# Optimization experiments

Measured on AMD Instinct MI355X. Metric: run time of the kernel, lower is better.

Reference implementation:

```python
import jax, jax.numpy as jnp
import numpy as np

C, HEADS, K, P, S = 384, 12, 3, 1, 1
B, H, W = 8, 56, 56


def _unfold(v, k, p, s):
    # v: [B, C, Hs, Ws] -> [B, C, k*k, oh*ow], matching torch.nn.Unfold layout
    b, c, hs, ws = v.shape
    vp = jnp.pad(v, ((0, 0), (0, 0), (p, p), (p, p)))
    oh = (hs + 2 * p - k) // s + 1
    ow = (ws + 2 * p - k) // s + 1
    patches = jnp.stack(
        [vp[:, :, i:i + oh * s:s, j:j + ow * s:s] for i in range(k) for j in range(k)],
        axis=2,
    )  # [B, C, k*k, oh, ow]
    return patches.reshape(b, c, k * k, oh * ow)


def _fold(patches, out_h, out_w, k, p, s):
    # patches: [B, C, k*k, oh, ow] -> scatter-add to [B, C, out_h, out_w]
    b, c, _, oh, ow = patches.shape
    out = jnp.zeros((b, c, out_h + 2 * p, out_w + 2 * p), patches.dtype)
    for i in range(k):
        for j in range(k):
            out = out.at[:, :, i:i + oh * s:s, j:j + ow * s:s].add(patches[:, :, i * k + j])
    return out[:, :, p:p + out_h, p:p + out_w]


def setup_inputs() -> dict:
    key = jax.random.key(0)
    ks = jax.random.split(key, 6)
    sc = C ** -0.5
    return {
        "x": jax.random.normal(ks[0], (B, C, H, W), jnp.float32),
        "Wv": jax.random.normal(ks[1], (C, C), jnp.float32) * sc,
        "Wa": jax.random.normal(ks[2], (K ** 4 * HEADS, C), jnp.float32) * sc,
        "ba": jax.random.normal(ks[3], (K ** 4 * HEADS,), jnp.float32) * 0.01,
        "Wp": jax.random.normal(ks[4], (C, C), jnp.float32) * sc,
        "bp": jax.random.normal(ks[5], (C,), jnp.float32) * 0.01,
    }


def reference(x, Wv, Wa, ba, Wp, bp):
    b, c, h, w = x.shape
    hd = c // HEADS
    height = -(-h // S)
    width = -(-w // S)
    L = height * width
    x_hwc = x.transpose(0, 2, 3, 1)  # [B,H,W,C]
    # value projection, then the original's spatial transpose quirk: [B,C,W,H]
    v = jnp.einsum('bhwc,dc->bdwh', x_hwc, Wv)
    v = _unfold(v, K, P, S)  # [B, C, k*k, L]
    v = v.reshape(b, HEADS, hd, K * K, L).transpose(0, 1, 4, 3, 2)  # [B,n,L,k2,hd]
    # avgPool with kernel=stride=1 is identity
    a = jnp.einsum('bhwc,ec->bhwe', x_hwc, Wa) + ba
    a = a.reshape(b, L, HEADS, K * K, K * K).transpose(0, 2, 1, 3, 4)
    a = jax.nn.softmax(a * (hd ** -0.5), axis=-1)  # [B,n,L,k2,k2]
    out = jnp.einsum('bnlpq,bnlqd->bnlpd', a, v)  # [B,n,L,k2,hd]
    out = out.transpose(0, 1, 4, 3, 2).reshape(b, c, K * K, height, width)
    out = _fold(out, h, w, K, P, S)  # [B,C,H,W]
    out = jnp.einsum('bchw,dc->bhwd', out, Wp) + bp
    return out.transpose(0, 3, 1, 2)
```

## Files before the change

kernel.cpp:

```cpp
#include <hip/hip_runtime.h>
#include <hip/hip_bf16.h>
#include <math.h>

#define BATCH 8
#define CIN   384
#define HEADS 12
#define HGT   56
#define WID   56
#define HW    3136
#define NPIX  (BATCH*HW)
#define NVAL  384
#define NATT_W 1152
#define NQKV  1536
#define KSTEPS (CIN/32)

typedef __bf16 bf16x8 __attribute__((ext_vector_type(8)));
typedef __bf16 bf16x4 __attribute__((ext_vector_type(4)));
typedef float f32x4 __attribute__((ext_vector_type(4)));
typedef __hip_bfloat16 hbf16;

__device__ __forceinline__ void gload_lds16(const void* g, void* l) {
  __builtin_amdgcn_global_load_lds(
      (const __attribute__((address_space(1))) void*)g,
      (__attribute__((address_space(3))) void*)l, 16, 0, 0);
}

#define NB_CONVX 9408
#define NB_WQKV  2304
#define NB_WP    576
__global__ __launch_bounds__(256) void prep_all(
    const float* __restrict__ x,
    const float* __restrict__ Wv, const float* __restrict__ Wa,
    const float* __restrict__ ba, const float* __restrict__ Wp,
    hbf16* __restrict__ xb, hbf16* __restrict__ wcat,
    float* __restrict__ bcat, hbf16* __restrict__ wpb)
{
  const int bid = blockIdx.x;
  const int tid = threadIdx.x;
  if (bid < NB_CONVX) {
    __shared__ float s[32][33];
    const int xt = bid % 98;
    const int yt = (bid / 98) % 12;
    const int b  = bid / (98 * 12);
    const int hw0 = xt * 32, c0 = yt * 32;
    const int tx = tid & 31, ty = tid >> 5;
    #pragma unroll
    for (int i = 0; i < 4; i++) {
      int c = c0 + ty + i * 8;
      s[ty + i * 8][tx] = x[((size_t)b * CIN + c) * HW + hw0 + tx];
    }
    __syncthreads();
    #pragma unroll
    for (int i = 0; i < 4; i++) {
      int hw = hw0 + ty + i * 8;
      xb[((size_t)b * HW + hw) * CIN + c0 + tx] =
          __float2bfloat16(s[tx][ty + i * 8]);
    }
  } else if (bid < NB_CONVX + NB_WQKV) {
    const int i = (bid - NB_CONVX) * 256 + tid;
    if (i < NQKV * CIN) {
      int n = i / CIN, k = i % CIN;
      float v = 0.f;
      if (n < NVAL) {
        v = Wv[(size_t)n * CIN + k];
      } else {
        int a = n - NVAL;
        int head = a / 96, r = a % 96, p = r / 10, q = r % 10;
        if (p < 9 && q < 9)
          v = Wa[(size_t)(head * 81 + p * 9 + q) * CIN + k];
      }
      wcat[i] = __float2bfloat16(v);
    }
    if (i < NQKV) {
      float bv = 0.f;
      if (i >= NVAL) {
        int a = i - NVAL;
        int head = a / 96, r = a % 96, p = r / 10, q = r % 10;
        if (p < 9 && q < 9) bv = ba[head * 81 + p * 9 + q];
      }
      bcat[i] = bv;
    }
  } else {
    const int i = (bid - NB_CONVX - NB_WQKV) * 256 + tid;
    if (i < CIN * CIN) wpb[i] = __float2bfloat16(Wp[i]);
  }
}

template<int MODE>
__global__ __launch_bounds__(256, 4) void gemm_fused(
    const hbf16* __restrict__ A_,
    const hbf16* __restrict__ Bt_,
    const float* __restrict__ bias,
    hbf16* __restrict__ ovp,
    hbf16* __restrict__ oat,
    float* __restrict__ oput)
{
  __shared__ __align__(16) char smem[33280];
  const __bf16* A  = (const __bf16*)A_;
  const __bf16* Bt = (const __bf16*)Bt_;

  const int tid  = threadIdx.x;
  const int wave = tid >> 6, lane = tid & 63;
  const int wr = wave >> 1, wc = wave & 1;
  const int l16 = lane & 15, kg = lane >> 4;
  const int m0 = blockIdx.x * 128, n0 = blockIdx.y * 128;

  float* biasLds = (float*)(smem + 32768);
  if (tid < 128) biasLds[tid] = bias[n0 + tid];

  const int srow = tid >> 2;
  const int skb  = (tid & 3) * 16;

  f32x4 acc[4][4] = {};

  auto stage = [&](int k0, int buf) {
    const char* gA = (const char*)(A  + (size_t)m0 * CIN + k0);
    const char* gB = (const char*)(Bt + (size_t)n0 * CIN + k0);
    char* lA = smem + buf * 16384;
    char* lB = smem + buf * 16384 + 8192;
    #pragma unroll
    for (int p = 0; p < 2; p++) {
      int row = p * 64 + srow;
      gload_lds16(gA + (size_t)row * (CIN * 2) + skb, lA + p * 4096 + wave * 1024);
      gload_lds16(gB + (size_t)row * (CIN * 2) + skb, lB + p * 4096 + wave * 1024);
    }
  };

  stage(0, 0);
  __syncthreads();

  for (int t = 0; t < KSTEPS; ++t) {
    const int buf = t & 1;
    if (t + 1 < KSTEPS) stage((t + 1) * 32, buf ^ 1);

    const __bf16* As = (const __bf16*)(smem + buf * 16384);
    const __bf16* Bs = (const __bf16*)(smem + buf * 16384 + 8192);
    bf16x8 af[4], bfr[4];
    #pragma unroll
    for (int mi = 0; mi < 4; mi++)
      af[mi] = *(const bf16x8*)(As + (wr * 64 + mi * 16 + l16) * 32 + kg * 8);
    #pragma unroll
    for (int ni = 0; ni < 4; ni++)
      bfr[ni] = *(const bf16x8*)(Bs + (wc * 64 + ni * 16 + l16) * 32 + kg * 8);
    #pragma unroll
    for (int mi = 0; mi < 4; mi++)
      #pragma unroll
      for (int ni = 0; ni < 4; ni++) {
        if (MODE == 0)
          acc[ni][mi] = __builtin_amdgcn_mfma_f32_16x16x32_bf16(
              bfr[ni], af[mi], acc[ni][mi], 0, 0, 0);
        else
          acc[mi][ni] = __builtin_amdgcn_mfma_f32_16x16x32_bf16(
              af[mi], bfr[ni], acc[mi][ni], 0, 0, 0);
      }
    __syncthreads();
  }

  if (MODE == 0) {
    __bf16* epi = (__bf16*)smem;
    #pragma unroll
    for (int ni = 0; ni < 4; ni++) {
      #pragma unroll
      for (int mi = 0; mi < 4; mi++) {
        const int m  = wr * 64 + mi * 16 + l16;
        const int nb = wc * 64 + ni * 16 + kg * 4;
        bf16x4 v4;
        #pragma unroll
        for (int r = 0; r < 4; r++)
          v4[r] = (__bf16)__float2bfloat16(acc[ni][mi][r] + biasLds[nb + r]);
        *(bf16x4*)(epi + m * 128 + (nb ^ ((m & 7) << 3))) = v4;
      }
    }
    __syncthreads();
    const bool isv = (n0 < NVAL);
    #pragma unroll
    for (int q = 0; q < 8; q++) {
      const int cid = q * 256 + tid;
      const int m = cid >> 4, nc = cid & 15;
      const int nloc = nc * 8;
      bf16x8 v = *(const bf16x8*)(epi + m * 128 + (nloc ^ ((m & 7) << 3)));
      const int mg = m0 + m;
      if (isv)
        *(bf16x8*)(ovp + (size_t)mg * NVAL + n0 + nloc) = v;
      else
        *(bf16x8*)(oat + (size_t)mg * NATT_W + (n0 - NVAL) + nloc) = v;
    }
  } else {
    float* epi = (float*)smem;
    #pragma unroll
    for (int p = 0; p < 2; p++) {
      if (p) __syncthreads();
      if (wr == p) {
        #pragma unroll
        for (int mi = 0; mi < 4; mi++) {
          #pragma unroll
          for (int ni = 0; ni < 4; ni++) {
            const int n  = wc * 64 + ni * 16 + l16;
            const int ml = mi * 16 + kg * 4;
            f32x4 v;
            #pragma unroll
            for (int r = 0; r < 4; r++) v[r] = acc[mi][ni][r] + biasLds[n];
            *(f32x4*)(epi + n * 64 + (ml ^ ((n & 7) << 2))) = v;
          }
        }
      }
      __syncthreads();
      #pragma unroll
      for (int q = 0; q < 8; q++) {
        const int cid = q * 256 + tid;
        const int n = cid >> 4, mc = cid & 15;
        const int ml = mc * 4;
        f32x4 v = *(const f32x4*)(epi + n * 64 + (ml ^ ((n & 7) << 2)));
        const int mg = m0 + p * 64 + ml;
        const int b = mg / HW, hw = mg % HW;
        *(f32x4*)(oput + ((size_t)b * NVAL + n0 + n) * HW + hw) = v;
      }
    }
  }
}

__global__ __launch_bounds__(256) void fold_fused(
    const hbf16* __restrict__ attnb,
    const hbf16* __restrict__ vprojb,
    hbf16* __restrict__ foldedb)
{
  __shared__ float Wl[4][4 * HEADS * 25];

  const int b    = blockIdx.x & 7;
  const int tile = blockIdx.x >> 3;
  const int tx = tile % 14, ty = tile / 14;
  const int bofs = b * HW;
  const int tid = threadIdx.x;
  const int w    = tid >> 6;
  const int lane = tid & 63;
  const int x0 = tx * 4 + (w & 1) * 2;
  const int y0 = ty * 4 + (w >> 1) * 2;
  const bool interior = (tx >= 1) && (tx <= 12) && (ty >= 1) && (ty <= 12);
  const float scale = 0.17677669529663687f;

  if (lane < 48) {
    const int pixL = lane / HEADS, head = lane - pixL * HEADS;
    const int y = y0 + (pixL >> 1), x = x0 + (pixL & 1);

    float W[25];
    #pragma unroll
    for (int k = 0; k < 25; k++) W[k] = 0.f;

    auto docenter = [&](int i, int j) {
      const uint32_t* rp = (const uint32_t*)(attnb +
          (size_t)(bofs + (y - i + 1) * WID + (x - j + 1)) * NATT_W +
          head * 96 + (i * 3 + j) * 10);
      float v[9];
      #pragma unroll
      for (int u = 0; u < 4; u++) {
        uint32_t bits = rp[u];
        v[2 * u]     = __uint_as_float(bits << 16) * scale;
        v[2 * u + 1] = __uint_as_float(bits & 0xffff0000u) * scale;
      }
      v[8] = __uint_as_float(rp[4] << 16) * scale;
      float m = -1e30f;
      #pragma unroll
      for (int q = 0; q < 9; q++) m = fmaxf(m, v[q]);
      float s = 0.f;
      #pragma unroll
      for (int q = 0; q < 9; q++) { v[q] = __expf(v[q] - m); s += v[q]; }
      const float inv = 1.f / s;
      #pragma unroll
      for (int ip = 0; ip < 3; ip++)
        #pragma unroll
        for (int jp = 0; jp < 3; jp++)
          W[(ip - i + 2) * 5 + (jp - j + 2)] += v[ip * 3 + jp] * inv;
    };

    if (interior) {
      #pragma unroll
      for (int i = 0; i < 3; i++)
        #pragma unroll
        for (int j = 0; j < 3; j++)
          docenter(i, j);
    } else {
      #pragma unroll
      for (int i = 0; i < 3; i++)
        #pragma unroll
        for (int j = 0; j < 3; j++) {
          const int hh = y - i + 1, ww = x - j + 1;
          if (hh >= 0 && hh < HGT && ww >= 0 && ww < WID) docenter(i, j);
        }
    }
    float* o = &Wl[w][(pixL * HEADS + head) * 25];
    #pragma unroll
    for (int k = 0; k < 25; k++) o[k] = W[k];
  }

  asm volatile("s_waitcnt lgkmcnt(0)" ::: "memory");
  __builtin_amdgcn_wave_barrier();

  const int pixL = lane >> 4;
  const int ch16 = lane & 15;
  const int y = y0 + (pixL >> 1), x = x0 + (pixL & 1);
  const size_t pixofs = (size_t)(bofs + y * WID + x);
  const hbf16* vb0 = vprojb + (size_t)(bofs + (x - 2) * WID + (y - 2)) * NVAL;

  #pragma unroll
  for (int it = 0; it < 3; it++) {
    const int c0 = ch16 * 8 + it * 128;
    const int head = c0 >> 5;
    const float* Wp = &Wl[w][(pixL * HEADS + head) * 25];
    float acc[8];
    #pragma unroll
    for (int k = 0; k < 8; k++) acc[k] = 0.f;

    if (interior) {
      #pragma unroll
      for (int a = 0; a < 5; a++)
        #pragma unroll
        for (int e = 0; e < 5; e++) {
          const float w_ = Wp[a * 5 + e];
          const uint32_t* v = (const uint32_t*)(vb0 + (e * WID + a) * NVAL + c0);
          uint32_t b0 = v[0], b1 = v[1], b2 = v[2], b3 = v[3];
          acc[0] += w_ * __uint_as_float(b0 << 16);
          acc[1] += w_ * __uint_as_float(b0 & 0xffff0000u);
          acc[2] += w_ * __uint_as_float(b1 << 16);
          acc[3] += w_ * __uint_as_float(b1 & 0xffff0000u);
          acc[4] += w_ * __uint_as_float(b2 << 16);
          acc[5] += w_ * __uint_as_float(b2 & 0xffff0000u);
          acc[6] += w_ * __uint_as_float(b3 << 16);
          acc[7] += w_ * __uint_as_float(b3 & 0xffff0000u);
        }
    } else {
      #pragma unroll
      for (int a = 0; a < 5; a++) {
        const int wi = y + a - 2;
        #pragma unroll
        for (int e = 0; e < 5; e++) {
          const int hi = x + e - 2;
          if (wi >= 0 && wi < WID && hi >= 0 && hi < HGT) {
            const float w_ = Wp[a * 5 + e];
            const uint32_t* v = (const uint32_t*)(
                vprojb + (size_t)(bofs + hi * WID + wi) * NVAL + c0);
            uint32_t b0 = v[0], b1 = v[1], b2 = v[2], b3 = v[3];
            acc[0] += w_ * __uint_as_float(b0 << 16);
            acc[1] += w_ * __uint_as_float(b0 & 0xffff0000u);
            acc[2] += w_ * __uint_as_float(b1 << 16);
            acc[3] += w_ * __uint_as_float(b1 & 0xffff0000u);
            acc[4] += w_ * __uint_as_float(b2 << 16);
            acc[5] += w_ * __uint_as_float(b2 & 0xffff0000u);
            acc[6] += w_ * __uint_as_float(b3 << 16);
            acc[7] += w_ * __uint_as_float(b3 & 0xffff0000u);
          }
        }
      }
    }

    bf16x8 o;
    #pragma unroll
    for (int k = 0; k < 8; k++) o[k] = (__bf16)__float2bfloat16(acc[k]);
    *(bf16x8*)(foldedb + pixofs * NVAL + c0) = o;
  }
}

extern "C" void kernel_launch(void* const* d_in, const int* in_sizes, int n_in,
                              void* d_out, int out_size, void* d_ws, size_t ws_size,
                              hipStream_t stream)
{
  const float* x  = (const float*)d_in[0];
  const float* Wv = (const float*)d_in[1];
  const float* Wa = (const float*)d_in[2];
  const float* ba = (const float*)d_in[3];
  const float* Wp = (const float*)d_in[4];
  const float* bp = (const float*)d_in[5];
  float* out = (float*)d_out;

  char* w = (char*)d_ws;
  const size_t ATTN_B  = (size_t)NPIX * NATT_W * 2;
  const size_t VPROJ_B = (size_t)NPIX * NVAL * 2;
  const size_t XB_B    = (size_t)NPIX * CIN * 2;
  hbf16* attnb  = (hbf16*)w;
  hbf16* vprojb = (hbf16*)(w + ATTN_B);
  hbf16* xb     = (hbf16*)(w + ATTN_B + VPROJ_B);
  hbf16* wcat   = (hbf16*)(w + ATTN_B + VPROJ_B + XB_B);
  hbf16* wpb    = wcat + (size_t)NQKV * CIN;
  float* bcat   = (float*)(wpb + (size_t)CIN * CIN);
  hbf16* foldedb = xb;

  prep_all<<<dim3(NB_CONVX + NB_WQKV + NB_WP), 256, 0, stream>>>(
      x, Wv, Wa, ba, Wp, xb, wcat, bcat, wpb);
  gemm_fused<0><<<dim3(NPIX / 128, NQKV / 128), 256, 0, stream>>>(
      xb, wcat, bcat, vprojb, attnb, nullptr);
  fold_fused<<<dim3(8 * 196), 256, 0, stream>>>(attnb, vprojb, foldedb);
  gemm_fused<1><<<dim3(NPIX / 128, NVAL / 128), 256, 0, stream>>>(
      foldedb, wpb, bp, nullptr, nullptr, out);
}
```

Measured before the change: 129.6 us.

## Swizzle GEMM block order and compute fold softmax per center pixel

The GEMM launches become 1D grids with a remapped block order: groups of 8 M-blocks sweep all N-blocks together, with a tail path for the leftover M-blocks. This is meant to improve L2 reuse of A tiles across XCDs. The fold kernel now computes each center pixel's 9 softmaxes once per 4x4 tile, using a 6x6 halo with vectorized 16-byte loads. Results are accumulated into a shared 16-pixel weight table with LDS atomics, replacing per-pixel recomputation of every neighbour's softmax. This cuts redundant global reads and exp work, at the cost of LDS zeroing, atomics and an extra block barrier.

New measurement: 228.3 us. 76.1% more time.

```diff
diff --git a/kernel.cpp b/kernel.cpp
--- a/kernel.cpp
+++ b/kernel.cpp
@@ -13,10 +13,12 @@
 #define NATT_W 1152
 #define NQKV  1536
 #define KSTEPS (CIN/32)
+#define MB_TOT 196
 
 typedef __bf16 bf16x8 __attribute__((ext_vector_type(8)));
 typedef __bf16 bf16x4 __attribute__((ext_vector_type(4)));
 typedef float f32x4 __attribute__((ext_vector_type(4)));
+typedef uint32_t u32x4 __attribute__((ext_vector_type(4)));
 typedef __hip_bfloat16 hbf16;
 
 __device__ __forceinline__ void gload_lds16(const void* g, void* l) {
@@ -103,7 +105,23 @@
   const int wave = tid >> 6, lane = tid & 63;
   const int wr = wave >> 1, wc = wave & 1;
   const int l16 = lane & 15, kg = lane >> 4;
-  const int m0 = blockIdx.x * 128, n0 = blockIdx.y * 128;
+
+  const int NBN   = (MODE == 0) ? (NQKV / 128) : (NVAL / 128);
+  const int FULLB = 8 * NBN * (MB_TOT / 8);
+  int mb, nb;
+  {
+    const int wgid = blockIdx.x;
+    if (wgid < FULLB) {
+      const int xc = wgid & 7, r = wgid >> 3;
+      nb = r % NBN;
+      mb = (r / NBN) * 8 + xc;
+    } else {
+      const int l = wgid - FULLB;
+      nb = l >> 2;
+      mb = (MB_TOT & ~7) + (l & 3);
+    }
+  }
+  const int m0 = mb * 128, n0 = nb * 128;
 
   float* biasLds = (float*)(smem + 32768);
   if (tid < 128) biasLds[tid] = bias[n0 + tid];
@@ -163,12 +181,12 @@
       #pragma unroll
       for (int mi = 0; mi < 4; mi++) {
         const int m  = wr * 64 + mi * 16 + l16;
-        const int nb = wc * 64 + ni * 16 + kg * 4;
+        const int nb2 = wc * 64 + ni * 16 + kg * 4;
         bf16x4 v4;
         #pragma unroll
         for (int r = 0; r < 4; r++)
-          v4[r] = (__bf16)__float2bfloat16(acc[ni][mi][r] + biasLds[nb + r]);
-        *(bf16x4*)(epi + m * 128 + (nb ^ ((m & 7) << 3))) = v4;
+          v4[r] = (__bf16)__float2bfloat16(acc[ni][mi][r] + biasLds[nb2 + r]);
+        *(bf16x4*)(epi + m * 128 + (nb2 ^ ((m & 7) << 3))) = v4;
       }
     }
     __syncthreads();
@@ -224,88 +242,79 @@
     const hbf16* __restrict__ vprojb,
     hbf16* __restrict__ foldedb)
 {
-  __shared__ float Wl[4][4 * HEADS * 25];
+  __shared__ float Wl[16 * HEADS * 25];
 
   const int b    = blockIdx.x & 7;
   const int tile = blockIdx.x >> 3;
   const int tx = tile % 14, ty = tile / 14;
+  const int x0 = tx * 4, y0 = ty * 4;
   const int bofs = b * HW;
   const int tid = threadIdx.x;
-  const int w    = tid >> 6;
-  const int lane = tid & 63;
-  const int x0 = tx * 4 + (w & 1) * 2;
-  const int y0 = ty * 4 + (w >> 1) * 2;
+  const float scale = 0.17677669529663687f;
+
+  for (int i = tid; i < 16 * HEADS * 25; i += 256) Wl[i] = 0.f;
+  __syncthreads();
+
+  for (int u = tid; u < 36 * HEADS; u += 256) {
+    const int cpL = u / HEADS, head = u - cpL * HEADS;
+    const int cy = y0 + (cpL / 6) - 1;
+    const int cx = x0 + (cpL % 6) - 1;
+    if (cy < 0 || cy >= HGT || cx < 0 || cx >= WID) continue;
+
+    const u32x4* base = (const u32x4*)(attnb +
+        (size_t)(bofs + cy * WID + cx) * NATT_W + head * 96);
+    u32x4 dv[12];
+    #pragma unroll
+    for (int k = 0; k < 12; k++) dv[k] = base[k];
+
+    #pragma unroll
+    for (int r = 0; r < 9; r++) {
+      const int i = r / 3, j = r % 3;
+      const int py = cy + i - 1, px = cx + j - 1;
+      if (py >= y0 && py < y0 + 4 && px >= x0 && px < x0 + 4) {
+        float v[9];
+        #pragma unroll
+        for (int t = 0; t < 4; t++) {
+          const int k = 5 * r + t;
+          const uint32_t bits = dv[k >> 2][k & 3];
+          v[2 * t]     = __uint_as_float(bits << 16) * scale;
+          v[2 * t + 1] = __uint_as_float(bits & 0xffff0000u) * scale;
+        }
+        {
+          const int k = 5 * r + 4;
+          v[8] = __uint_as_float(dv[k >> 2][k & 3] << 16) * scale;
+        }
+        float m = -1e30f;
+        #pragma unroll
+        for (int q = 0; q < 9; q++) m = fmaxf(m, v[q]);
+        float s = 0.f;
+        #pragma unroll
+        for (int q = 0; q < 9; q++) { v[q] = __expf(v[q] - m); s += v[q]; }
+        const float inv = 1.f / s;
+        const int pixL = (py - y0) * 4 + (px - x0);
+        float* wp = &Wl[(pixL * HEADS + head) * 25];
+        #pragma unroll
+        for (int ip = 0; ip < 3; ip++)
+          #pragma unroll
+          for (int jp = 0; jp < 3; jp++)
+            atomicAdd(&wp[(ip - i + 2) * 5 + (jp - j + 2)], v[ip * 3 + jp] * inv);
+      }
+    }
+  }
+  __syncthreads();
+
+  const int pixL = tid >> 4;
+  const int ch16 = tid & 15;
+  const int y = y0 + (pixL >> 2), x = x0 + (pixL & 3);
+  const size_t pixofs = (size_t)(bofs + y * WID + x);
   const bool interior = (tx >= 1) && (tx <= 12) && (ty >= 1) && (ty <= 12);
-  const float scale = 0.17677669529663687f;
-
-  if (lane < 48) {
-    const int pixL = lane / HEADS, head = lane - pixL * HEADS;
-    const int y = y0 + (pixL >> 1), x = x0 + (pixL & 1);
-
-    float W[25];
-    #pragma unroll
-    for (int k = 0; k < 25; k++) W[k] = 0.f;
-
-    auto docenter = [&](int i, int j) {
-      const uint32_t* rp = (const uint32_t*)(attnb +
-          (size_t)(bofs + (y - i + 1) * WID + (x - j + 1)) * NATT_W +
-          head * 96 + (i * 3 + j) * 10);
-      float v[9];
-      #pragma unroll
-      for (int u = 0; u < 4; u++) {
-        uint32_t bits = rp[u];
-        v[2 * u]     = __uint_as_float(bits << 16) * scale;
-        v[2 * u + 1] = __uint_as_float(bits & 0xffff0000u) * scale;
-      }
-      v[8] = __uint_as_float(rp[4] << 16) * scale;
-      float m = -1e30f;
-      #pragma unroll
-      for (int q = 0; q < 9; q++) m = fmaxf(m, v[q]);
-      float s = 0.f;
-      #pragma unroll
-      for (int q = 0; q < 9; q++) { v[q] = __expf(v[q] - m); s += v[q]; }
-      const float inv = 1.f / s;
-      #pragma unroll
-      for (int ip = 0; ip < 3; ip++)
-        #pragma unroll
-        for (int jp = 0; jp < 3; jp++)
-          W[(ip - i + 2) * 5 + (jp - j + 2)] += v[ip * 3 + jp] * inv;
-    };
-
-    if (interior) {
-      #pragma unroll
-      for (int i = 0; i < 3; i++)
-        #pragma unroll
-        for (int j = 0; j < 3; j++)
-          docenter(i, j);
-    } else {
-      #pragma unroll
-      for (int i = 0; i < 3; i++)
-        #pragma unroll
-        for (int j = 0; j < 3; j++) {
-          const int hh = y - i + 1, ww = x - j + 1;
-          if (hh >= 0 && hh < HGT && ww >= 0 && ww < WID) docenter(i, j);
-        }
-    }
-    float* o = &Wl[w][(pixL * HEADS + head) * 25];
-    #pragma unroll
-    for (int k = 0; k < 25; k++) o[k] = W[k];
-  }
-
-  asm volatile("s_waitcnt lgkmcnt(0)" ::: "memory");
-  __builtin_amdgcn_wave_barrier();
-
-  const int pixL = lane >> 4;
-  const int ch16 = lane & 15;
-  const int y = y0 + (pixL >> 1), x = x0 + (pixL & 1);
-  const size_t pixofs = (size_t)(bofs + y * WID + x);
   const hbf16* vb0 = vprojb + (size_t)(bofs + (x - 2) * WID + (y - 2)) * NVAL;
 
   #pragma unroll
   for (int it = 0; it < 3; it++) {
     const int c0 = ch16 * 8 + it * 128;
     const int head = c0 >> 5;
-    const float* Wp = &Wl[w][(pixL * HEADS + head) * 25];
+    const float* Wp = &Wl[(pixL * HEADS + head) * 25];
     float acc[8];
     #pragma unroll
     for (int k = 0; k < 8; k++) acc[k] = 0.f;
@@ -385,9 +394,9 @@
 
   prep_all<<<dim3(NB_CONVX + NB_WQKV + NB_WP), 256, 0, stream>>>(
       x, Wv, Wa, ba, Wp, xb, wcat, bcat, wpb);
-  gemm_fused<0><<<dim3(NPIX / 128, NQKV / 128), 256, 0, stream>>>(
+  gemm_fused<0><<<dim3(MB_TOT * (NQKV / 128)), 256, 0, stream>>>(
       xb, wcat, bcat, vprojb, attnb, nullptr);
   fold_fused<<<dim3(8 * 196), 256, 0, stream>>>(attnb, vprojb, foldedb);
-  gemm_fused<1><<<dim3(NPIX / 128, NVAL / 128), 256, 0, stream>>>(
+  gemm_fused<1><<<dim3(MB_TOT * (NVAL / 128)), 256, 0, stream>>>(
       foldedb, wpb, bp, nullptr, nullptr, out);
 }
```

## Remap GEMM workgroups for XCD locality and widen fold tile to whole block

Applied to the files above, without the earlier changes.

The GEMM launches become a 1D grid with a custom block-id mapping that groups 8 consecutive M-blocks with all N-blocks, likely so that workgroups sharing A rows land on the same XCD/L2. The fold kernel now lets one block process a 4x4 pixel tile: 192 threads compute the softmax-fold weights for all 16 pixels, and the block uses a __syncthreads instead of per-wave 2x2 tiles. This shares the weight computation across the block, at the cost of idling 64 threads during the weight phase and adding a block-wide barrier.

After: 121.6 us. -6.2%, faster.

```diff
diff --git a/kernel.cpp b/kernel.cpp
--- a/kernel.cpp
+++ b/kernel.cpp
@@ -13,6 +13,7 @@
 #define NATT_W 1152
 #define NQKV  1536
 #define KSTEPS (CIN/32)
+#define MB_TOT 196
 
 typedef __bf16 bf16x8 __attribute__((ext_vector_type(8)));
 typedef __bf16 bf16x4 __attribute__((ext_vector_type(4)));
@@ -103,7 +104,23 @@
   const int wave = tid >> 6, lane = tid & 63;
   const int wr = wave >> 1, wc = wave & 1;
   const int l16 = lane & 15, kg = lane >> 4;
-  const int m0 = blockIdx.x * 128, n0 = blockIdx.y * 128;
+
+  const int NBN   = (MODE == 0) ? (NQKV / 128) : (NVAL / 128);
+  const int FULLB = 8 * NBN * (MB_TOT / 8);
+  int mb, nb;
+  {
+    const int wgid = blockIdx.x;
+    if (wgid < FULLB) {
+      const int xc = wgid & 7, r = wgid >> 3;
+      nb = r % NBN;
+      mb = (r / NBN) * 8 + xc;
+    } else {
+      const int l = wgid - FULLB;
+      nb = l >> 2;
+      mb = (MB_TOT & ~7) + (l & 3);
+    }
+  }
+  const int m0 = mb * 128, n0 = nb * 128;
 
   float* biasLds = (float*)(smem + 32768);
   if (tid < 128) biasLds[tid] = bias[n0 + tid];
@@ -163,12 +180,12 @@
       #pragma unroll
       for (int mi = 0; mi < 4; mi++) {
         const int m  = wr * 64 + mi * 16 + l16;
-        const int nb = wc * 64 + ni * 16 + kg * 4;
+        const int nb2 = wc * 64 + ni * 16 + kg * 4;
         bf16x4 v4;
         #pragma unroll
         for (int r = 0; r < 4; r++)
-          v4[r] = (__bf16)__float2bfloat16(acc[ni][mi][r] + biasLds[nb + r]);
-        *(bf16x4*)(epi + m * 128 + (nb ^ ((m & 7) << 3))) = v4;
+          v4[r] = (__bf16)__float2bfloat16(acc[ni][mi][r] + biasLds[nb2 + r]);
+        *(bf16x4*)(epi + m * 128 + (nb2 ^ ((m & 7) << 3))) = v4;
       }
     }
     __syncthreads();
@@ -224,23 +241,20 @@
     const hbf16* __restrict__ vprojb,
     hbf16* __restrict__ foldedb)
 {
-  __shared__ float Wl[4][4 * HEADS * 25];
+  __shared__ float Wl[16 * HEADS * 25];
 
   const int b    = blockIdx.x & 7;
   const int tile = blockIdx.x >> 3;
   const int tx = tile % 14, ty = tile / 14;
+  const int x0 = tx * 4, y0 = ty * 4;
   const int bofs = b * HW;
   const int tid = threadIdx.x;
-  const int w    = tid >> 6;
-  const int lane = tid & 63;
-  const int x0 = tx * 4 + (w & 1) * 2;
-  const int y0 = ty * 4 + (w >> 1) * 2;
   const bool interior = (tx >= 1) && (tx <= 12) && (ty >= 1) && (ty <= 12);
   const float scale = 0.17677669529663687f;
 
-  if (lane < 48) {
-    const int pixL = lane / HEADS, head = lane - pixL * HEADS;
-    const int y = y0 + (pixL >> 1), x = x0 + (pixL & 1);
+  if (tid < 192) {
+    const int pixL = tid / HEADS, head = tid - pixL * HEADS;
+    const int y = y0 + (pixL >> 2), x = x0 + (pixL & 3);
 
     float W[25];
     #pragma unroll
@@ -287,17 +301,15 @@
           if (hh >= 0 && hh < HGT && ww >= 0 && ww < WID) docenter(i, j);
         }
     }
-    float* o = &Wl[w][(pixL * HEADS + head) * 25];
+    float* o = &Wl[tid * 25];
     #pragma unroll
     for (int k = 0; k < 25; k++) o[k] = W[k];
   }
-
-  asm volatile("s_waitcnt lgkmcnt(0)" ::: "memory");
-  __builtin_amdgcn_wave_barrier();
-
-  const int pixL = lane >> 4;
-  const int ch16 = lane & 15;
-  const int y = y0 + (pixL >> 1), x = x0 + (pixL & 1);
+  __syncthreads();
+
+  const int pixL = tid >> 4;
+  const int ch16 = tid & 15;
+  const int y = y0 + (pixL >> 2), x = x0 + (pixL & 3);
   const size_t pixofs = (size_t)(bofs + y * WID + x);
   const hbf16* vb0 = vprojb + (size_t)(bofs + (x - 2) * WID + (y - 2)) * NVAL;
 
@@ -305,7 +317,7 @@
   for (int it = 0; it < 3; it++) {
     const int c0 = ch16 * 8 + it * 128;
     const int head = c0 >> 5;
-    const float* Wp = &Wl[w][(pixL * HEADS + head) * 25];
+    const float* Wp = &Wl[(pixL * HEADS + head) * 25];
     float acc[8];
     #pragma unroll
     for (int k = 0; k < 8; k++) acc[k] = 0.f;
@@ -385,9 +397,9 @@
 
   prep_all<<<dim3(NB_CONVX + NB_WQKV + NB_WP), 256, 0, stream>>>(
       x, Wv, Wa, ba, Wp, xb, wcat, bcat, wpb);
-  gemm_fused<0><<<dim3(NPIX / 128, NQKV / 128), 256, 0, stream>>>(
+  gemm_fused<0><<<dim3(MB_TOT * (NQKV / 128)), 256, 0, stream>>>(
       xb, wcat, bcat, vprojb, attnb, nullptr);
   fold_fused<<<dim3(8 * 196), 256, 0, stream>>>(attnb, vprojb, foldedb);
-  gemm_fused<1><<<dim3(NPIX / 128, NVAL / 128), 256, 0, stream>>>(
+  gemm_fused<1><<<dim3(MB_TOT * (NVAL / 128)), 256, 0, stream>>>(
       foldedb, wpb, bp, nullptr, nullptr, out);
 }
```
